# Optimization experiments

Measured on AMD Instinct MI355X. Metric: run time of the kernel, lower is better.

## Reference

```python
import jax, jax.numpy as jnp
import numpy as np

N_CLASSES = 3
FEAT_SIZES = (64, 32)  # source1 64x64, source2 32x32 for 512x512 input


def conv(x, w, b):
    # x: NCHW, w: OIHW, 3x3 SAME, stride 1
    y = jax.lax.conv_general_dilated(
        x, w, window_strides=(1, 1), padding='SAME',
        dimension_numbers=('NCHW', 'OIHW', 'NCHW'))
    return y + b[None, :, None, None]


def maxpool(x):
    return jax.lax.reduce_window(x, -jnp.inf, jax.lax.max,
                                 (1, 1, 2, 2), (1, 1, 2, 2), 'VALID')


def l2norm(x, gamma, eps=1e-10):
    # standard SSD L2Norm: per-position channel L2 normalize, learned per-channel scale
    n = jnp.sqrt(jnp.sum(x * x, axis=1, keepdims=True)) + eps
    return gamma[None, :, None, None] * x / n


def make_priors():
    # PriorBox: one prior per feature-map cell, normalized (cx, cy) centers
    ps = []
    for f in FEAT_SIZES:
        c = (jnp.arange(f, dtype=jnp.float32) + 0.5) / f
        cy, cx = jnp.meshgrid(c, c, indexing='ij')
        ps.append(jnp.stack([cx.ravel(), cy.ravel()], axis=1))  # [f*f, 2]
    return jnp.concatenate(ps, axis=0)  # [5120, 2]


def setup_inputs() -> dict:
    key = jax.random.key(0)
    ks = iter(jax.random.split(key, 32))

    def he(k, shape):
        fan_in = shape[1] * shape[2] * shape[3]
        return jax.random.normal(k, shape, jnp.float32) * (2.0 / fan_in) ** 0.5

    d = {'x': jax.random.normal(next(ks), (8, 2, 512, 512), jnp.float32)}
    shapes = [(64, 2, 3, 3), (64, 64, 3, 3), (128, 64, 3, 3), (128, 128, 3, 3),
              (256, 128, 3, 3), (256, 256, 3, 3), (256, 256, 3, 3), (256, 256, 3, 3)]
    for n, s in enumerate(shapes, 1):
        d[f'w{n}'] = he(next(ks), s)
        d[f'b{n}'] = jnp.zeros((s[0],), jnp.float32)
    d['g1'] = 20.0 * jnp.ones((256,), jnp.float32)  # L2Norm1 weight
    d['g2'] = 20.0 * jnp.ones((256,), jnp.float32)  # L2Norm2 weight
    for pre, oc in (('l', 2), ('c', N_CLASSES), ('r', 1)):
        for si in (1, 2):
            d[f'{pre}w{si}'] = he(next(ks), (oc, 256, 3, 3))
            d[f'{pre}b{si}'] = jnp.zeros((oc,), jnp.float32)
    return d


def reference(x, w1, b1, w2, b2, w3, b3, w4, b4, w5, b5, w6, b6, w7, b7, w8, b8,
              g1, g2, lw1, lb1, lw2, lb2, cw1, cb1, cw2, cb2, rw1, rb1, rw2, rb2):
    B = x.shape[0]
    r = jax.nn.relu
    # vgg[0:33]
    x = r(conv(x, w1, b1)); x = r(conv(x, w2, b2)); x = maxpool(x)
    x = r(conv(x, w3, b3)); x = r(conv(x, w4, b4)); x = maxpool(x)
    x = r(conv(x, w5, b5)); x = r(conv(x, w6, b6)); x = maxpool(x)
    s1 = l2norm(x, g1)                 # [B,256,64,64]
    # vgg[33:]
    x = maxpool(x)
    x = r(conv(x, w7, b7)); x = r(conv(x, w8, b8))
    s2 = l2norm(x, g2)                 # [B,256,32,32]

    def head(s, w_, b_):
        # conv -> permute(0,2,3,1) -> flatten, as in the torch forward
        return conv(s, w_, b_).transpose(0, 2, 3, 1).reshape(B, -1)

    loc = jnp.concatenate([head(s1, lw1, lb1), head(s2, lw2, lb2)], 1).reshape(B, -1, 2)
    conf = jnp.concatenate([head(s1, cw1, cb1), head(s2, cw2, cb2)], 1).reshape(B, -1, N_CLASSES)
    regr = jnp.concatenate([head(s1, rw1, rb1), head(s2, rw2, rb2)], 1).reshape(B, -1, 1)
    priors = make_priors()
    return loc, conf, regr, priors
```

## Files before the change

### kernel.cpp

```cpp
#include <hip/hip_runtime.h>

typedef _Float16 f16;
typedef _Float16 f16x8 __attribute__((ext_vector_type(8)));
typedef float f32x4 __attribute__((ext_vector_type(4)));

__device__ __forceinline__ f32x4 mfma16(f16x8 a, f16x8 b, f32x4 c) {
    return __builtin_amdgcn_mfma_f32_16x16x32_f16(a, b, c, 0, 0, 0);
}

template<int IC, int OC, int BX, int WY, int WO, int MT, int NT, bool POOL>
__global__ __launch_bounds__(256) void convmf_k(
    const f16* __restrict__ in, const f16* __restrict__ wt,
    const float* __restrict__ bias, f16* __restrict__ out,
    int H, int W, int ocBlocks, long inStride, long outStride)
{
    constexpr int WROWS = MT * 16 / BX;
    constexpr int BROWS = WROWS * WY;
    constexpr int SR = BROWS + 2;
    constexpr int SC = BX + 2;
    constexpr int LOG = (BX == 64) ? 6 : 5;
    static_assert(!POOL || (BX == 64 && MT == 8), "pool path assumes BX==64, MT==8");
    __shared__ f16 lds[SR * SC * 40];

    const int tid  = threadIdx.x;
    const int lane = tid & 63;
    const int wv   = tid >> 6;
    const int wy   = wv / WO;
    const int wo   = wv % WO;
    const int lm   = lane & 15;
    const int lk   = lane >> 4;
    const int x0   = blockIdx.x * BX;
    const int y0   = blockIdx.y * BROWS;
    const int zb   = blockIdx.z;
    const int n    = zb / ocBlocks;
    const int oc0  = (zb - n * ocBlocks) * (16 * NT * WO) + wo * (16 * NT);
    in  += (long)n * inStride;
    out += (long)n * outStride;

    f32x4 acc[MT][NT];
#pragma unroll
    for (int mt = 0; mt < MT; ++mt)
#pragma unroll
        for (int nt = 0; nt < NT; ++nt)
            acc[mt][nt] = (f32x4){0.f, 0.f, 0.f, 0.f};

    const int Wp = W + 2;
    for (int ic0 = 0; ic0 < IC; ic0 += 32) {
        if (ic0) __syncthreads();
        const f16* ip = in + ((long)y0 * Wp + x0) * IC + ic0;
        constexpr int TASKS = SR * SC * 4;
        for (int s = tid; s < TASKS; s += 256) {
            int r    = s / (SC * 4);
            int rem  = s - r * (SC * 4);
            int xcol = rem >> 2;
            int g    = rem & 3;
            f16x8 v = *(const f16x8*)(ip + ((long)r * Wp + xcol) * IC + g * 8);
            *(f16x8*)&lds[(r * SC + xcol) * 40 + g * 8] = v;
        }
        __syncthreads();

        for (int t = 0; t < 9; ++t) {
            int dy = t / 3, dx = t - dy * 3;
            const f16* wp = wt + ((long)t * OC + oc0) * IC + ic0 + lk * 8;
            f16x8 bfr[NT];
#pragma unroll
            for (int nt = 0; nt < NT; ++nt)
                bfr[nt] = *(const f16x8*)(wp + (nt * 16 + lm) * IC);
#pragma unroll
            for (int mt = 0; mt < MT; ++mt) {
                int pos = mt * 16 + lm;
                int xx = pos & (BX - 1);
                int yy = wy * WROWS + (pos >> LOG);
                f16x8 a = *(const f16x8*)&lds[((yy + dy) * SC + xx + dx) * 40 + lk * 8];
#pragma unroll
                for (int nt = 0; nt < NT; ++nt)
                    acc[mt][nt] = mfma16(a, bfr[nt], acc[mt][nt]);
            }
        }
    }

    if constexpr (!POOL) {
#pragma unroll
        for (int nt = 0; nt < NT; ++nt) {
            int oc = oc0 + nt * 16 + lm;
            float bs = bias[oc];
#pragma unroll
            for (int mt = 0; mt < MT; ++mt) {
#pragma unroll
                for (int r = 0; r < 4; ++r) {
                    int pos = mt * 16 + lk * 4 + r;
                    int xx = pos & (BX - 1);
                    int yy = wy * WROWS + (pos >> LOG);
                    float v = fmaxf(acc[mt][nt][r] + bs, 0.f);
                    out[((long)(y0 + yy + 1) * (W + 2) + (x0 + xx + 1)) * OC + oc] = (f16)v;
                }
            }
        }
    } else {
        const int Wo = W >> 1;
#pragma unroll
        for (int nt = 0; nt < NT; ++nt) {
            int oc = oc0 + nt * 16 + lm;
            float bs = bias[oc];
#pragma unroll
            for (int mt = 0; mt < 4; ++mt) {
#pragma unroll
                for (int r = 0; r < 4; r += 2) {
                    float v = fmaxf(fmaxf(acc[mt][nt][r], acc[mt][nt][r + 1]),
                                    fmaxf(acc[mt + 4][nt][r], acc[mt + 4][nt][r + 1]));
                    v = fmaxf(v + bs, 0.f);
                    int pos = mt * 16 + lk * 4 + r;
                    int xo = pos >> 1;
                    out[((long)((y0 >> 1) + wy + 1) * (Wo + 2) + ((x0 >> 1) + xo + 1)) * OC + oc] = (f16)v;
                }
            }
        }
    }
}

__global__ __launch_bounds__(256) void convmf1_k(
    const float* __restrict__ x, int itemBase,
    const f16* __restrict__ wt1,
    const float* __restrict__ bias, f16* __restrict__ out, long outStride)
{
    __shared__ f16 ldsx[10 * 66 * 2];
    __shared__ f16 ldsa[512 * 40];
    const int tid = threadIdx.x;
    const int lane = tid & 63;
    const int wv = tid >> 6;
    const int lm = lane & 15;
    const int lk = lane >> 4;
    const int x0 = blockIdx.x * 64;
    const int y0 = blockIdx.y * 8;
    const float* xb = x + (long)(itemBase + blockIdx.z) * 2 * 512 * 512;
    out += (long)blockIdx.z * outStride;

    for (int s = tid; s < 660; s += 256) {
        int r = s / 66, xc = s - r * 66;
        int gy = y0 + r - 1, gx = x0 + xc - 1;
        f16 v0 = (f16)0.f, v1 = (f16)0.f;
        if ((unsigned)gy < 512u && (unsigned)gx < 512u) {
            v0 = (f16)xb[(long)gy * 512 + gx];
            v1 = (f16)xb[262144 + (long)gy * 512 + gx];
        }
        ldsx[(r * 66 + xc) * 2]     = v0;
        ldsx[(r * 66 + xc) * 2 + 1] = v1;
    }
    __syncthreads();
    for (int s = tid; s < 2048; s += 256) {
        int pos = s >> 2, g = s & 3;
        int row = pos >> 6, col = pos & 63;
        f16x8 v;
#pragma unroll
        for (int j = 0; j < 8; ++j) {
            int k = g * 8 + j;
            f16 val = (f16)0.f;
            if (k < 18) {
                int t = k >> 1, ic = k & 1;
                int dy = t / 3, dx = t - dy * 3;
                val = ldsx[((row + dy) * 66 + col + dx) * 2 + ic];
            }
            v[j] = val;
        }
        *(f16x8*)&ldsa[pos * 40 + g * 8] = v;
    }
    __syncthreads();

    f32x4 acc[8][4];
#pragma unroll
    for (int mt = 0; mt < 8; ++mt)
#pragma unroll
        for (int nt = 0; nt < 4; ++nt)
            acc[mt][nt] = (f32x4){0.f, 0.f, 0.f, 0.f};

    f16x8 b0 = *(const f16x8*)(wt1 + (0 * 16 + lm) * 32 + lk * 8);
    f16x8 b1 = *(const f16x8*)(wt1 + (1 * 16 + lm) * 32 + lk * 8);
    f16x8 b2 = *(const f16x8*)(wt1 + (2 * 16 + lm) * 32 + lk * 8);
    f16x8 b3 = *(const f16x8*)(wt1 + (3 * 16 + lm) * 32 + lk * 8);
#pragma unroll
    for (int mt = 0; mt < 8; ++mt) {
        int pos = wv * 128 + mt * 16 + lm;
        f16x8 a = *(const f16x8*)&ldsa[pos * 40 + lk * 8];
        acc[mt][0] = mfma16(a, b0, acc[mt][0]);
        acc[mt][1] = mfma16(a, b1, acc[mt][1]);
        acc[mt][2] = mfma16(a, b2, acc[mt][2]);
        acc[mt][3] = mfma16(a, b3, acc[mt][3]);
    }
#pragma unroll
    for (int nt = 0; nt < 4; ++nt) {
        int oc = nt * 16 + lm;
        float bs = bias[oc];
#pragma unroll
        for (int mt = 0; mt < 8; ++mt) {
#pragma unroll
            for (int r = 0; r < 4; ++r) {
                int pos = wv * 128 + mt * 16 + lk * 4 + r;
                int xx = pos & 63, yy = pos >> 6;
                float v = fmaxf(acc[mt][nt][r] + bs, 0.f);
                out[((long)(y0 + yy + 1) * 514 + (x0 + xx + 1)) * 64 + oc] = (f16)v;
            }
        }
    }
}

template<int BX>
__global__ __launch_bounds__(256) void headconv_k(
    const f16* __restrict__ s, long sStride, const f16* __restrict__ wth,
    const float* __restrict__ lb, const float* __restrict__ cb, const float* __restrict__ rb,
    float* __restrict__ loc, float* __restrict__ conf, float* __restrict__ regr,
    int W, int posoff)
{
    constexpr int BY = (BX == 64) ? 1 : 2;
    constexpr int SR = BY + 2, SC = BX + 2;
    constexpr int LOG = (BX == 64) ? 6 : 5;
    __shared__ f16 lds[SR * SC * 40];
    const int tid = threadIdx.x;
    const int lane = tid & 63;
    const int wv = tid >> 6;
    const int lm = lane & 15;
    const int lk = lane >> 4;
    const int y0 = blockIdx.y * BY;
    const int b = blockIdx.z;
    s += (long)b * sStride;

    f32x4 acc = (f32x4){0.f, 0.f, 0.f, 0.f};
    const int Wp = W + 2;
    for (int ic0 = 0; ic0 < 256; ic0 += 32) {
        if (ic0) __syncthreads();
        const f16* ip = s + (long)y0 * Wp * 256 + ic0;
        constexpr int TASKS = SR * SC * 4;
        for (int t = tid; t < TASKS; t += 256) {
            int r = t / (SC * 4);
            int rem = t - r * (SC * 4);
            int xcol = rem >> 2, g = rem & 3;
            f16x8 v = *(const f16x8*)(ip + ((long)r * Wp + xcol) * 256 + g * 8);
            *(f16x8*)&lds[(r * SC + xcol) * 40 + g * 8] = v;
        }
        __syncthreads();
        for (int t = 0; t < 9; ++t) {
            int dy = t / 3, dx = t - dy * 3;
            f16x8 bf = *(const f16x8*)(wth + ((long)t * 16 + lm) * 256 + ic0 + lk * 8);
            int pos = wv * 16 + lm;
            int xx = pos & (BX - 1), yy = pos >> LOG;
            f16x8 a = *(const f16x8*)&lds[((yy + dy) * SC + xx + dx) * 40 + lk * 8];
            acc = mfma16(a, bf, acc);
        }
    }
#pragma unroll
    for (int r = 0; r < 4; ++r) {
        int pos = wv * 16 + lk * 4 + r;
        int xx = pos & (BX - 1), yy = pos >> LOG;
        int P = posoff + (y0 + yy) * W + xx;
        float v = acc[r];
        if (lm < 2)       loc[((long)b * 5120 + P) * 2 + lm]       = v + lb[lm];
        else if (lm < 5)  conf[((long)b * 5120 + P) * 3 + (lm - 2)] = v + cb[lm - 2];
        else if (lm == 5) regr[(long)b * 5120 + P]                  = v + rb[0];
    }
}

__global__ __launch_bounds__(256) void cvt_wt_k(const float* __restrict__ w, f16* __restrict__ wt,
                                                int OC, int IC)
{
    int idx = blockIdx.x * 256 + threadIdx.x;
    if (idx >= OC * IC) return;
    int oc = idx / IC, ic = idx - oc * IC;
#pragma unroll
    for (int t = 0; t < 9; ++t)
        wt[((long)t * OC + oc) * IC + ic] = (f16)w[(long)idx * 9 + t];
}

__global__ __launch_bounds__(64) void cvt_wt1_k(const float* __restrict__ w, f16* __restrict__ wt1)
{
    int oc = threadIdx.x;
#pragma unroll
    for (int k = 0; k < 32; ++k) {
        f16 v = (f16)0.f;
        if (k < 18) {
            int t = k >> 1, ic = k & 1;
            v = (f16)w[((long)oc * 2 + ic) * 9 + t];
        }
        wt1[oc * 32 + k] = v;
    }
}

__global__ __launch_bounds__(256) void cvt_wth_k(const float* __restrict__ lw, const float* __restrict__ cw,
                                                 const float* __restrict__ rw, f16* __restrict__ wth)
{
    int idx = blockIdx.x * 256 + threadIdx.x;
    if (idx >= 9 * 16 * 256) return;
    int t = idx / (16 * 256);
    int r = (idx / 256) & 15;
    int ic = idx & 255;
    float v = 0.f;
    if (r < 2)      v = lw[((long)r * 256 + ic) * 9 + t];
    else if (r < 5) v = cw[((long)(r - 2) * 256 + ic) * 9 + t];
    else if (r == 5) v = rw[(long)ic * 9 + t];
    wth[((long)t * 16 + r) * 256 + ic] = (f16)v;
}

__global__ __launch_bounds__(256) void halo_k(f16* __restrict__ buf, int W, int H, int C,
                                              long stride, int items)
{
    int per = (2 * (W + 2) + 2 * H) * C;
    long total = (long)per * items;
    long idx = (long)blockIdx.x * 256 + threadIdx.x;
    if (idx >= total) return;
    int n = idx / per;
    int j = idx - (long)n * per;
    int c = j % C, p = j / C;
    int row, col;
    if (p < W + 2) { row = 0; col = p; }
    else if (p < 2 * (W + 2)) { row = H + 1; col = p - (W + 2); }
    else { int q = p - 2 * (W + 2); row = 1 + (q >> 1); col = (q & 1) ? (W + 1) : 0; }
    buf[(long)n * stride + ((long)row * (W + 2) + col) * C + c] = (f16)0.f;
}

__global__ __launch_bounds__(256) void l2n_k(const f16* __restrict__ in, const float* __restrict__ g,
                                             f16* __restrict__ out, int W, long stride, int total)
{
    int i = blockIdx.x * 256 + threadIdx.x;
    if (i >= total) return;
    int b = i / (W * W);
    int rem = i - b * W * W;
    int y = rem / W, x = rem - y * W;
    long off = (long)b * stride + ((long)(y + 1) * (W + 2) + x + 1) * 256;
    const f16* p = in + off;
    f16* q = out + off;
    float s = 0.f;
    for (int gg = 0; gg < 32; ++gg) {
        f16x8 v = *(const f16x8*)(p + gg * 8);
#pragma unroll
        for (int j = 0; j < 8; ++j) { float f = (float)v[j]; s = fmaf(f, f, s); }
    }
    float inv = 1.f / (sqrtf(s) + 1e-10f);
    for (int gg = 0; gg < 32; ++gg) {
        f16x8 v = *(const f16x8*)(p + gg * 8);
        f16x8 o;
#pragma unroll
        for (int j = 0; j < 8; ++j) o[j] = (f16)(g[gg * 8 + j] * ((float)v[j] * inv));
        *(f16x8*)(q + gg * 8) = o;
    }
}

__global__ __launch_bounds__(256) void mp_k(const f16* __restrict__ in, f16* __restrict__ out)
{
    int idx = blockIdx.x * 256 + threadIdx.x;
    if (idx >= 8 * 32 * 32 * 32) return;
    int gg = idx & 31;
    int xo = (idx >> 5) & 31;
    int yo = (idx >> 10) & 31;
    int b = idx >> 15;
    const f16* p = in + (long)b * 1115136 + ((long)(2 * yo + 1) * 66 + 2 * xo + 1) * 256 + gg * 8;
    f16x8 a0 = *(const f16x8*)p;
    f16x8 a1 = *(const f16x8*)(p + 256);
    f16x8 a2 = *(const f16x8*)(p + 66 * 256);
    f16x8 a3 = *(const f16x8*)(p + 66 * 256 + 256);
    f16x8 o;
#pragma unroll
    for (int j = 0; j < 8; ++j)
        o[j] = (f16)fmaxf(fmaxf((float)a0[j], (float)a1[j]), fmaxf((float)a2[j], (float)a3[j]));
    *(f16x8*)(out + (long)b * 295936 + ((long)(yo + 1) * 34 + xo + 1) * 256 + gg * 8) = o;
}

__global__ __launch_bounds__(256) void priors_k(float* __restrict__ out)
{
    int r = blockIdx.x * 256 + threadIdx.x;
    if (r >= 5120) return;
    float cx, cy;
    if (r < 4096) {
        int i = r >> 6, j = r & 63;
        cx = (j + 0.5f) / 64.0f; cy = (i + 0.5f) / 64.0f;
    } else {
        int rr = r - 4096;
        int i = rr >> 5, j = rr & 31;
        cx = (j + 0.5f) / 32.0f; cy = (i + 0.5f) / 32.0f;
    }
    out[2 * r] = cx;
    out[2 * r + 1] = cy;
}

extern "C" void kernel_launch(void* const* d_in, const int* in_sizes, int n_in,
                              void* d_out, int out_size, void* d_ws, size_t ws_size,
                              hipStream_t stream)
{
    const float* x  = (const float*)d_in[0];
    const float* w1 = (const float*)d_in[1];  const float* b1 = (const float*)d_in[2];
    const float* w2 = (const float*)d_in[3];  const float* b2 = (const float*)d_in[4];
    const float* w3 = (const float*)d_in[5];  const float* b3 = (const float*)d_in[6];
    const float* w4 = (const float*)d_in[7];  const float* b4 = (const float*)d_in[8];
    const float* w5 = (const float*)d_in[9];  const float* b5 = (const float*)d_in[10];
    const float* w6 = (const float*)d_in[11]; const float* b6 = (const float*)d_in[12];
    const float* w7 = (const float*)d_in[13]; const float* b7 = (const float*)d_in[14];
    const float* w8 = (const float*)d_in[15]; const float* b8 = (const float*)d_in[16];
    const float* g1 = (const float*)d_in[17]; const float* g2 = (const float*)d_in[18];
    const float* lw1 = (const float*)d_in[19]; const float* lb1 = (const float*)d_in[20];
    const float* lw2 = (const float*)d_in[21]; const float* lb2 = (const float*)d_in[22];
    const float* cw1 = (const float*)d_in[23]; const float* cb1 = (const float*)d_in[24];
    const float* cw2 = (const float*)d_in[25]; const float* cb2 = (const float*)d_in[26];
    const float* rw1 = (const float*)d_in[27]; const float* rb1 = (const float*)d_in[28];
    const float* rw2 = (const float*)d_in[29]; const float* rb2 = (const float*)d_in[30];

    f16* wsh = (f16*)d_ws;
    f16* wt2  = wsh + 0;
    f16* wt3  = wsh + 36864;
    f16* wt4  = wsh + 110592;
    f16* wt5  = wsh + 258048;
    f16* wt6  = wsh + 552960;
    f16* wt7  = wsh + 1142784;
    f16* wt8  = wsh + 1732608;
    f16* wt1  = wsh + 2322432;
    f16* wth1 = wsh + 2324480;
    f16* wth2 = wsh + 2361344;
    f16* x6p  = wsh + 2398208;
    const long PI = 11319296;

    const long A1S = 16908544;
    const long P1S = 4260096;
    const long A3S = 8520192;
    const long P2S = 2163200;
    const long A5S = 4326400;
    const long PH2 = 18391040;

    int G = 1;
    for (int g = 8; g >= 1; g >>= 1) {
        long ext = (long)g * (A1S + P1S); if (ext < PH2) ext = PH2;
        if (2.0 * (double)(PI + ext) <= (double)ws_size) { G = g; break; }
    }
    const int NGRP = 8 / G;

    f16* a1 = wsh + PI;
    f16* p1 = wsh + PI + (long)G * A1S;
    f16* a3 = a1;
    f16* p2 = p1;
    f16* a5 = a1;
    f16* s1 = wsh + PI;
    f16* p4 = wsh + PI + 8921088;
    f16* a7 = wsh + PI + 11288576;
    f16* a8 = wsh + PI + 13656064;
    f16* s2 = wsh + PI + 16023552;

    float* loc  = (float*)d_out;
    float* conf = loc + 81920;
    float* regr = loc + 204800;
    float* pri  = loc + 245760;

    cvt_wt_k<<<dim3((64 * 64 + 255) / 256), 256, 0, stream>>>(w2, wt2, 64, 64);
    cvt_wt_k<<<dim3((128 * 64 + 255) / 256), 256, 0, stream>>>(w3, wt3, 128, 64);
    cvt_wt_k<<<dim3((128 * 128 + 255) / 256), 256, 0, stream>>>(w4, wt4, 128, 128);
    cvt_wt_k<<<dim3((256 * 128 + 255) / 256), 256, 0, stream>>>(w5, wt5, 256, 128);
    cvt_wt_k<<<dim3((256 * 256 + 255) / 256), 256, 0, stream>>>(w6, wt6, 256, 256);
    cvt_wt_k<<<dim3((256 * 256 + 255) / 256), 256, 0, stream>>>(w7, wt7, 256, 256);
    cvt_wt_k<<<dim3((256 * 256 + 255) / 256), 256, 0, stream>>>(w8, wt8, 256, 256);
    cvt_wt1_k<<<dim3(1), 64, 0, stream>>>(w1, wt1);
    cvt_wth_k<<<dim3(144), 256, 0, stream>>>(lw1, cw1, rw1, wth1);
    cvt_wth_k<<<dim3(144), 256, 0, stream>>>(lw2, cw2, rw2, wth2);

    for (int grp = 0; grp < NGRP; ++grp) {
        f16* x6g = x6p + (long)grp * G * 1115136;
        halo_k<<<dim3((G * (2 * 514 + 2 * 512) * 64 + 255) / 256), 256, 0, stream>>>(a1, 512, 512, 64, A1S, G);
        halo_k<<<dim3((G * (2 * 258 + 2 * 256) * 64 + 255) / 256), 256, 0, stream>>>(p1, 256, 256, 64, P1S, G);
        convmf1_k<<<dim3(8, 64, G), 256, 0, stream>>>(x, grp * G, wt1, b1, a1, A1S);
        convmf_k<64, 64, 64, 2, 2, 8, 2, true><<<dim3(8, 128, G), 256, 0, stream>>>(
            a1, wt2, b2, p1, 512, 512, 1, A1S, P1S);
        halo_k<<<dim3((G * (2 * 258 + 2 * 256) * 128 + 255) / 256), 256, 0, stream>>>(a3, 256, 256, 128, A3S, G);
        convmf_k<64, 128, 64, 2, 2, 8, 2, false><<<dim3(4, 64, 2 * G), 256, 0, stream>>>(
            p1, wt3, b3, a3, 256, 256, 2, P1S, A3S);
        halo_k<<<dim3((G * (2 * 130 + 2 * 128) * 128 + 255) / 256), 256, 0, stream>>>(p2, 128, 128, 128, P2S, G);
        convmf_k<128, 128, 64, 2, 2, 8, 2, true><<<dim3(4, 64, 2 * G), 256, 0, stream>>>(
            a3, wt4, b4, p2, 256, 256, 2, A3S, P2S);
        halo_k<<<dim3((G * (2 * 130 + 2 * 128) * 256 + 255) / 256), 256, 0, stream>>>(a5, 128, 128, 256, A5S, G);
        convmf_k<128, 256, 64, 2, 2, 8, 2, false><<<dim3(2, 32, 4 * G), 256, 0, stream>>>(
            p2, wt5, b5, a5, 128, 128, 4, P2S, A5S);
        convmf_k<256, 256, 64, 2, 2, 8, 2, true><<<dim3(2, 32, 4 * G), 256, 0, stream>>>(
            a5, wt6, b6, x6g, 128, 128, 4, A5S, 1115136);
    }

    halo_k<<<dim3((8 * (2 * 66 + 2 * 64) * 256 + 255) / 256), 256, 0, stream>>>(s1, 64, 64, 256, 1115136, 8);
    halo_k<<<dim3((8 * (2 * 34 + 2 * 32) * 256 + 255) / 256), 256, 0, stream>>>(p4, 32, 32, 256, 295936, 8);
    halo_k<<<dim3((8 * (2 * 34 + 2 * 32) * 256 + 255) / 256), 256, 0, stream>>>(a7, 32, 32, 256, 295936, 8);
    halo_k<<<dim3((8 * (2 * 34 + 2 * 32) * 256 + 255) / 256), 256, 0, stream>>>(s2, 32, 32, 256, 295936, 8);

    l2n_k<<<dim3((32768 + 255) / 256), 256, 0, stream>>>(x6p, g1, s1, 64, 1115136, 32768);
    mp_k<<<dim3((262144 + 255) / 256), 256, 0, stream>>>(x6p, p4);
    convmf_k<256, 256, 32, 2, 2, 4, 4, false><<<dim3(1, 8, 16), 256, 0, stream>>>(
        p4, wt7, b7, a7, 32, 32, 2, 295936, 295936);
    convmf_k<256, 256, 32, 2, 2, 4, 4, false><<<dim3(1, 8, 16), 256, 0, stream>>>(
        a7, wt8, b8, a8, 32, 32, 2, 295936, 295936);
    l2n_k<<<dim3((8192 + 255) / 256), 256, 0, stream>>>(a8, g2, s2, 32, 295936, 8192);

    headconv_k<64><<<dim3(1, 64, 8), 256, 0, stream>>>(
        s1, 1115136, wth1, lb1, cb1, rb1, loc, conf, regr, 64, 0);
    headconv_k<32><<<dim3(1, 16, 8), 256, 0, stream>>>(
        s2, 295936, wth2, lb2, cb2, rb2, loc, conf, regr, 32, 4096);
    priors_k<<<dim3(20), 256, 0, stream>>>(pri);

    (void)in_sizes; (void)n_in; (void)out_size; (void)ws_size;
}
```

Measured before the change: 1.178 ms.

## Stage conv input tiles with direct global-to-LDS loads and XOR-swizzled layout

```diff
diff --git a/kernel.cpp b/kernel.cpp
--- a/kernel.cpp
+++ b/kernel.cpp
@@ -19,8 +19,11 @@
     constexpr int SR = BROWS + 2;
     constexpr int SC = BX + 2;
     constexpr int LOG = (BX == 64) ? 6 : 5;
+    constexpr int NPIX = SR * SC;
+    constexpr int TASKS = NPIX * 4;
+    constexpr int TPAD = ((TASKS + 63) / 64) * 64;
     static_assert(!POOL || (BX == 64 && MT == 8), "pool path assumes BX==64, MT==8");
-    __shared__ f16 lds[SR * SC * 40];
+    __shared__ f16 lds[TPAD * 8];
 
     const int tid  = threadIdx.x;
     const int lane = tid & 63;
@@ -48,15 +51,22 @@
     for (int ic0 = 0; ic0 < IC; ic0 += 32) {
         if (ic0) __syncthreads();
         const f16* ip = in + ((long)y0 * Wp + x0) * IC + ic0;
-        constexpr int TASKS = SR * SC * 4;
-        for (int s = tid; s < TASKS; s += 256) {
-            int r    = s / (SC * 4);
-            int rem  = s - r * (SC * 4);
-            int xcol = rem >> 2;
-            int g    = rem & 3;
-            f16x8 v = *(const f16x8*)(ip + ((long)r * Wp + xcol) * IC + g * 8);
-            *(f16x8*)&lds[(r * SC + xcol) * 40 + g * 8] = v;
-        }
+        for (int s0 = 0; s0 < TPAD; s0 += 256) {
+            int base = s0 + wv * 64;
+            if (base < TASKS) {
+                int q = base + lane;
+                int p = q >> 2;
+                int g = (q & 3) ^ ((p >> 1) & 3);
+                int r = p / SC, xcol = p - r * SC;
+                long off = ((long)r * Wp + xcol) * IC + g * 8;
+                if (q >= TASKS) off = 0;
+                __builtin_amdgcn_global_load_lds(
+                    (const __attribute__((address_space(1))) void*)(ip + off),
+                    (__attribute__((address_space(3))) void*)&lds[(long)base * 8],
+                    16, 0, 0);
+            }
+        }
+        asm volatile("s_waitcnt vmcnt(0)" ::: "memory");
         __syncthreads();
 
         for (int t = 0; t < 9; ++t) {
@@ -71,7 +81,9 @@
                 int pos = mt * 16 + lm;
                 int xx = pos & (BX - 1);
                 int yy = wy * WROWS + (pos >> LOG);
-                f16x8 a = *(const f16x8*)&lds[((yy + dy) * SC + xx + dx) * 40 + lk * 8];
+                int pp = (yy + dy) * SC + xx + dx;
+                int slot = pp * 4 + (lk ^ ((pp >> 1) & 3));
+                f16x8 a = *(const f16x8*)&lds[slot * 8];
 #pragma unroll
                 for (int nt = 0; nt < NT; ++nt)
                     acc[mt][nt] = mfma16(a, bfr[nt], acc[mt][nt]);
```

New measurement: 1.255 ms. +6.5%, slower.
